# Optimization experiments

Measured on AMD Instinct MI355X. Metric: run time of the kernel, lower is better.

The kernel has to match this reference:

```python
import jax, jax.numpy as jnp
import numpy as np

GAMMA = 0.96875
HIDDEN = 512
BATCH = 4
SEQ = 2048


def setup_inputs() -> dict:
    key = jax.random.key(0)
    k1, k2, k3, k4, k5 = jax.random.split(key, 5)
    x = jax.random.normal(k1, (BATCH, SEQ, HIDDEN), dtype=jnp.float32)
    weight_q = jax.random.normal(k2, (HIDDEN, HIDDEN), dtype=jnp.float32) / HIDDEN
    weight_k = jax.random.normal(k3, (HIDDEN, HIDDEN), dtype=jnp.float32) / HIDDEN
    weight_v = jax.random.normal(k4, (HIDDEN, HIDDEN), dtype=jnp.float32) / HIDDEN
    theta = jax.random.normal(k5, (HIDDEN,), dtype=jnp.float32) / HIDDEN
    return {"x": x, "weight_q": weight_q, "weight_k": weight_k, "weight_v": weight_v, "theta": theta}


def reference(x, weight_q, weight_k, weight_v, theta):
    # x: [B, S, H] float32 -> complex64 parallel retention output [B, S, H]
    B, S, H = x.shape
    cplx = jnp.complex64
    # thetas[n-1] = exp(i * n * theta), n = 1..S  -> [S, H]
    n = jnp.arange(1, S + 1, dtype=jnp.float32)
    phase = n[:, None] * theta[None, :]
    thetas = jnp.exp(1j * phase.astype(cplx))
    xc = x.astype(cplx)
    q = (xc @ weight_q.astype(cplx)) * thetas[None]          # [B, S, H]
    k = (xc @ weight_k.astype(cplx)) * jnp.conj(thetas)[None]
    v = xc @ weight_v.astype(cplx)
    # decay mask D[i, j] = gamma^(i - j) for i >= j else 0   -> [S, S]
    idx = jnp.arange(S)
    diff = idx[:, None] - idx[None, :]
    D = jnp.where(diff >= 0, GAMMA ** jnp.maximum(diff, 0).astype(jnp.float32), 0.0)
    scores = jnp.einsum("bqh,bkh->bqk", q, k) * D.astype(cplx)  # [B, S, S] complex64
    out = jnp.einsum("bqk,bkh->bqh", scores, v)                 # [B, S, H] complex64
    return out
```

## Files before the change

### kernel.cpp

```cpp
#include <hip/hip_runtime.h>
#include <stdint.h>

#define LOG2G -0.045803689611862786f

typedef float f32x4 __attribute__((ext_vector_type(4)));
typedef short bf16x8 __attribute__((ext_vector_type(8)));

__device__ inline unsigned short f2bf(float f) {
  uint32_t u = __builtin_bit_cast(uint32_t, f);
  u += 0x7FFFu + ((u >> 16) & 1u);
  return (unsigned short)(u >> 16);
}
__device__ inline float b2f(unsigned short u) {
  return __builtin_bit_cast(float, (uint32_t)u << 16);
}

#if __has_builtin(__builtin_amdgcn_global_load_lds)
#define USE_GLL 1
#endif

__device__ __forceinline__ void stage_row(const unsigned short* __restrict__ srcrow,
                                          unsigned short* ldsrow, int lane, int swz) {
#ifdef USE_GLL
  __builtin_amdgcn_global_load_lds(
      (const __attribute__((address_space(1))) uint32_t*)((const char*)srcrow + ((lane ^ swz) << 4)),
      (__attribute__((address_space(3))) uint32_t*)ldsrow, 16, 0, 0);
#else
  bf16x8 v = *(const bf16x8*)((const char*)srcrow + ((lane ^ swz) << 4));
  *(bf16x8*)((char*)ldsrow + (lane << 4)) = v;
#endif
}

__global__ __launch_bounds__(256) void prep_kernel(
    const float* __restrict__ wq, const float* __restrict__ wk,
    const float* __restrict__ wv, unsigned short* __restrict__ Wt)
{
  __shared__ unsigned short lh[64][68];
  const int blk = blockIdx.x;
  const int w3 = blk >> 6;
  const int tile = blk & 63;
  const int tk = (tile >> 3) * 64, tn = (tile & 7) * 64;
  const float* W = (w3 == 0) ? wq : ((w3 == 1) ? wk : wv);
  const int t = threadIdx.x;
  {
    const int kl = t >> 2, nq = (t & 3) * 16;
#pragma unroll
    for (int f = 0; f < 4; ++f) {
      float4 v = *(const float4*)&W[(size_t)(tk + kl) * 512 + tn + nq + f * 4];
      float vv[4] = {v.x, v.y, v.z, v.w};
      ushort4 h4;
#pragma unroll
      for (int e = 0; e < 4; ++e) ((unsigned short*)&h4)[e] = f2bf(vv[e]);
      *(ushort4*)&lh[kl][nq + f * 4] = h4;
    }
  }
  __syncthreads();
  {
    const int nl = t >> 2, kq = (t & 3) * 16;
    unsigned short* outh = Wt + (size_t)w3 * 262144 + (size_t)(tn + nl) * 512 + tk + kq;
#pragma unroll
    for (int f = 0; f < 4; ++f) {
      ushort4 h4;
#pragma unroll
      for (int e = 0; e < 4; ++e) ((unsigned short*)&h4)[e] = lh[kq + f * 4 + e][nl];
      *(ushort4*)&outh[f * 4] = h4;
    }
  }
}

__global__ __launch_bounds__(256) void xconv_kernel(
    const float* __restrict__ x, unsigned short* __restrict__ xb)
{
  const size_t i = ((size_t)blockIdx.x * 256 + threadIdx.x) * 8;
  float4 v0 = *(const float4*)&x[i];
  float4 v1 = *(const float4*)&x[i + 4];
  bf16x8 o;
  o[0] = (short)f2bf(v0.x); o[1] = (short)f2bf(v0.y);
  o[2] = (short)f2bf(v0.z); o[3] = (short)f2bf(v0.w);
  o[4] = (short)f2bf(v1.x); o[5] = (short)f2bf(v1.y);
  o[6] = (short)f2bf(v1.z); o[7] = (short)f2bf(v1.w);
  *(bf16x8*)&xb[i] = o;
}

__global__ __launch_bounds__(256) void proj_kernel(
    const unsigned short* __restrict__ xb, const unsigned short* __restrict__ Wt,
    const float* __restrict__ theta,
    unsigned short* __restrict__ Qc, unsigned short* __restrict__ Qs,
    unsigned short* __restrict__ Kc, unsigned short* __restrict__ Ks,
    unsigned short* __restrict__ Vt)
{
  __shared__ unsigned short Al[64 * 512];
  __shared__ unsigned short Bl[64 * 512];
  __shared__ unsigned short T[64][136];
  const int tid = threadIdx.x;
  const int wave = tid >> 6, lane = tid & 63;
  const int r = lane & 15, g = lane >> 4;
  const int wm = wave >> 1, wn = wave & 1;
  const int nbase = blockIdx.x * 64, mbase = blockIdx.y * 64;

#pragma unroll
  for (int i = 0; i < 16; ++i) {
    const int row = wave * 16 + i;
    stage_row(xb + (size_t)(mbase + row) * 512, &Al[row * 512], lane, row & 7);
  }
#pragma unroll
  for (int i = 0; i < 16; ++i) {
    const int row = wave * 16 + i;
    stage_row(Wt + (size_t)(nbase + row) * 512, &Bl[row * 512], lane, row & 7);
  }

  float C1[2], S1[2], CZ[2], SZ[2], C16[2], S16[2];
  const int pos0 = (mbase & 2047) + wm * 32 + g * 4;
#pragma unroll
  for (int nf = 0; nf < 2; ++nf) {
    const float th = theta[nbase + wn * 32 + nf * 16 + r];
    float c1, s1, cz, sz;
    sincosf(th, &s1, &c1);
    sincosf((float)(pos0 + 1) * th, &sz, &cz);
    float c2 = c1 * c1 - s1 * s1, s2 = 2.f * c1 * s1;
    float c4 = c2 * c2 - s2 * s2, s4 = 2.f * c2 * s2;
    float c8 = c4 * c4 - s4 * s4, s8 = 2.f * c4 * s4;
    C1[nf] = c1; S1[nf] = s1; CZ[nf] = cz; SZ[nf] = sz;
    C16[nf] = c8 * c8 - s8 * s8; S16[nf] = 2.f * c8 * s8;
  }
  __syncthreads();

#pragma unroll
  for (int z = 0; z < 3; ++z) {
    f32x4 acc[2][2];
#pragma unroll
    for (int mf = 0; mf < 2; ++mf)
#pragma unroll
      for (int nf = 0; nf < 2; ++nf) acc[mf][nf] = (f32x4){0.f, 0.f, 0.f, 0.f};
#pragma unroll
    for (int ks = 0; ks < 16; ++ks) {
      const int off = (((ks * 4) + g) ^ (r & 7)) << 3;
      bf16x8 a0 = *(const bf16x8*)&Al[(wm * 32 + r) * 512 + off];
      bf16x8 a1 = *(const bf16x8*)&Al[(wm * 32 + 16 + r) * 512 + off];
      bf16x8 b0 = *(const bf16x8*)&Bl[(wn * 32 + r) * 512 + off];
      bf16x8 b1 = *(const bf16x8*)&Bl[(wn * 32 + 16 + r) * 512 + off];
      acc[0][0] = __builtin_amdgcn_mfma_f32_16x16x32_bf16(a0, b0, acc[0][0], 0, 0, 0);
      acc[0][1] = __builtin_amdgcn_mfma_f32_16x16x32_bf16(a0, b1, acc[0][1], 0, 0, 0);
      acc[1][0] = __builtin_amdgcn_mfma_f32_16x16x32_bf16(a1, b0, acc[1][0], 0, 0, 0);
      acc[1][1] = __builtin_amdgcn_mfma_f32_16x16x32_bf16(a1, b1, acc[1][1], 0, 0, 0);
    }
    __syncthreads();

    if (z < 2) {
#pragma unroll
      for (int i = 0; i < 16; ++i) {
        const int row = wave * 16 + i;
        stage_row(Wt + (size_t)(z + 1) * 262144 + (size_t)(nbase + row) * 512,
                  &Bl[row * 512], lane, row & 7);
      }
    }

    if (z == 2) {
#pragma unroll
      for (int nf = 0; nf < 2; ++nf) {
        const int nl = wn * 32 + nf * 16 + r;
#pragma unroll
        for (int mf = 0; mf < 2; ++mf)
#pragma unroll
          for (int i = 0; i < 4; ++i)
            T[nl][wm * 32 + mf * 16 + g * 4 + i] = f2bf(acc[mf][nf][i]);
      }
      __syncthreads();
      const int bb = mbase >> 11, posb = mbase & 2047;
#pragma unroll
      for (int p = 0; p < 2; ++p) {
        const int row = p * 32 + (tid >> 3);
        bf16x8 v = *(const bf16x8*)&T[row][(tid & 7) * 8];
        *(bf16x8*)&Vt[((size_t)bb * 512 + nbase + row) * 2048 + posb + (tid & 7) * 8] = v;
      }
    } else {
#pragma unroll
      for (int pl = 0; pl < 2; ++pl) {
        if (pl) __syncthreads();
#pragma unroll
        for (int nf = 0; nf < 2; ++nf) {
          const int nl = wn * 32 + nf * 16 + r;
          float cz = CZ[nf], sz = SZ[nf];
          const float c1 = C1[nf], s1 = S1[nf], c16 = C16[nf], s16 = S16[nf];
#pragma unroll
          for (int mf = 0; mf < 2; ++mf) {
            float cc = cz, ss = sz;
#pragma unroll
            for (int i = 0; i < 4; ++i) {
              const float f = pl ? ss : cc;
              T[wm * 32 + mf * 16 + g * 4 + i][nl] = f2bf(acc[mf][nf][i] * f);
              float nc = cc * c1 - ss * s1, ns = cc * s1 + ss * c1;
              cc = nc; ss = ns;
            }
            float zc = cz * c16 - sz * s16, zs = cz * s16 + sz * c16;
            cz = zc; sz = zs;
          }
        }
        __syncthreads();
        unsigned short* dst = (z == 0) ? (pl ? Qs : Qc) : (pl ? Ks : Kc);
#pragma unroll
        for (int p = 0; p < 2; ++p) {
          const int row = p * 32 + (tid >> 3);
          bf16x8 v = *(const bf16x8*)&T[row][(tid & 7) * 8];
          *(bf16x8*)&dst[(size_t)(mbase + row) * 512 + nbase + (tid & 7) * 8] = v;
        }
      }
      __syncthreads();
    }
  }
}

__global__ __launch_bounds__(256, 1) void ret_kernel(
    const unsigned short* __restrict__ Qc, const unsigned short* __restrict__ Qs,
    const unsigned short* __restrict__ Kc, const unsigned short* __restrict__ Ks,
    const unsigned short* __restrict__ Vt, uint32_t* __restrict__ out)
{
  __shared__ unsigned short Klds[64 * 512];
  __shared__ unsigned short Prl[2][16 * 40];
  __shared__ unsigned short Pil[2][16 * 40];

  const int bid = blockIdx.x;
  const int sid = ((bid & 7) << 5) + (bid >> 3);
  const int b = sid >> 6;
  const int qblk = 63 - (sid & 63);
  const int q0 = qblk * 32;
  const int tid = threadIdx.x;
  const int wave = tid >> 6;
  const int lane = tid & 63;
  const int r = lane & 15;
  const int g = lane >> 4;
  const int mf = wave & 1;
  const int wq = wave >> 1;
  const int sw = r & 7;

  bf16x8 qa[16], qb[16];
  {
    const unsigned short* qcr = Qc + ((size_t)b * 2048 + q0 + wq * 16 + r) * 512 + g * 8;
    const unsigned short* qsr = Qs + ((size_t)b * 2048 + q0 + wq * 16 + r) * 512 + g * 8;
#pragma unroll
    for (int ks = 0; ks < 16; ++ks) {
      qa[ks] = *(const bf16x8*)(qcr + ks * 32);
      qb[ks] = *(const bf16x8*)(qsr + ks * 32);
    }
  }
#pragma unroll
  for (int ks = 0; ks < 16; ++ks)
    asm volatile("" : "+v"(qa[ks]), "+v"(qb[ks]));

  const int ntiles = ((q0 + 31) >> 5) + 1;
  const int t0 = (q0 >= 256) ? ((q0 - 256) >> 5) : 0;

  {
    const size_t kbase = ((size_t)b * 2048 + (t0 << 5)) * 512;
#pragma unroll
    for (int i = 0; i < 16; ++i) {
      const int rid = wave * 16 + i;
      const int row = rid & 31;
      const unsigned short* src = ((rid < 32) ? Kc : Ks) + kbase + (size_t)row * 512;
      stage_row(src, &Klds[(size_t)rid * 512], lane, rid & 7);
    }
  }
  __syncthreads();

  f32x4 outre[2][8], outim[2][8];
#pragma unroll
  for (int qg = 0; qg < 2; ++qg)
#pragma unroll
    for (int c = 0; c < 8; ++c) {
      outre[qg][c] = (f32x4){0.f, 0.f, 0.f, 0.f};
      outim[qg][c] = (f32x4){0.f, 0.f, 0.f, 0.f};
    }

  for (int t = t0; t < ntiles; ++t) {
    const int m0 = t << 5;
    f32x4 acc_cc = {0.f, 0.f, 0.f, 0.f};
    f32x4 acc_ss = {0.f, 0.f, 0.f, 0.f};
    f32x4 ai1 = {0.f, 0.f, 0.f, 0.f};
    f32x4 ai2 = {0.f, 0.f, 0.f, 0.f};
    const unsigned short* krow_c = &Klds[(mf * 16 + r) * 512];
    const unsigned short* krow_s = krow_c + 32 * 512;
#pragma unroll
    for (int ks = 0; ks < 16; ++ks) {
      const int off = (((ks * 4) + g) ^ sw) << 3;
      bf16x8 ka = *(const bf16x8*)(krow_c + off);
      bf16x8 kb = *(const bf16x8*)(krow_s + off);
      acc_cc = __builtin_amdgcn_mfma_f32_16x16x32_bf16(ka, qa[ks], acc_cc, 0, 0, 0);
      acc_ss = __builtin_amdgcn_mfma_f32_16x16x32_bf16(kb, qb[ks], acc_ss, 0, 0, 0);
      ai1    = __builtin_amdgcn_mfma_f32_16x16x32_bf16(ka, qb[ks], ai1, 0, 0, 0);
      ai2    = __builtin_amdgcn_mfma_f32_16x16x32_bf16(kb, qa[ks], ai2, 0, 0, 0);
    }
    {
      const int qrow = q0 + wq * 16 + r;
      const int mg = m0 + mf * 16 + g * 4;
      ushort4 pkre, pkim;
#pragma unroll
      for (int rg = 0; rg < 4; ++rg) {
        int d = qrow - (mg + rg);
        float wdec = (d >= 0) ? exp2f((float)d * LOG2G) : 0.0f;
        ((unsigned short*)&pkre)[rg] = f2bf((acc_cc[rg] + acc_ss[rg]) * wdec);
        ((unsigned short*)&pkim)[rg] = f2bf((ai1[rg] - ai2[rg]) * wdec);
      }
      *(ushort4*)&Prl[wq][r * 40 + mf * 16 + g * 4] = pkre;
      *(ushort4*)&Pil[wq][r * 40 + mf * 16 + g * 4] = pkim;
    }
    __syncthreads();

    const unsigned short* vtp =
        Vt + ((size_t)b * 512 + wave * 128 + r) * 2048 + m0 + g * 8;
    bf16x8 vv[8];
#pragma unroll
    for (int c = 0; c < 8; ++c)
      vv[c] = *(const bf16x8*)(vtp + (size_t)c * 16 * 2048);

    if (t + 1 < ntiles) {
      const size_t kbase = ((size_t)b * 2048 + m0 + 32) * 512;
#pragma unroll
      for (int i = 0; i < 16; ++i) {
        const int rid = wave * 16 + i;
        const int row = rid & 31;
        const unsigned short* src = ((rid < 32) ? Kc : Ks) + kbase + (size_t)row * 512;
        stage_row(src, &Klds[(size_t)rid * 512], lane, rid & 7);
      }
    }

#pragma unroll
    for (int qg = 0; qg < 2; ++qg) {
      bf16x8 pr = *(const bf16x8*)&Prl[qg][r * 40 + g * 8];
      bf16x8 pi = *(const bf16x8*)&Pil[qg][r * 40 + g * 8];
#pragma unroll
      for (int c = 0; c < 8; ++c) {
        outre[qg][c] = __builtin_amdgcn_mfma_f32_16x16x32_bf16(pr, vv[c], outre[qg][c], 0, 0, 0);
        outim[qg][c] = __builtin_amdgcn_mfma_f32_16x16x32_bf16(pi, vv[c], outim[qg][c], 0, 0, 0);
      }
    }
    __syncthreads();
  }

#pragma unroll
  for (int qg = 0; qg < 2; ++qg)
#pragma unroll
    for (int c = 0; c < 8; ++c)
#pragma unroll
      for (int rg = 0; rg < 4; ++rg) {
        const int q = q0 + qg * 16 + g * 4 + rg;
        const int h = wave * 128 + c * 16 + r;
        const size_t o = ((size_t)b * 2048 + q) * 512 + h;
        out[o] = (uint32_t)f2bf(outim[qg][c][rg]) | ((uint32_t)f2bf(outre[qg][c][rg]) << 16);
      }
}

extern "C" void kernel_launch(void* const* d_in, const int* in_sizes, int n_in,
                              void* d_out, int out_size, void* d_ws, size_t ws_size,
                              hipStream_t stream) {
  (void)in_sizes; (void)n_in; (void)out_size; (void)ws_size;
  const float* x     = (const float*)d_in[0];
  const float* wq    = (const float*)d_in[1];
  const float* wk    = (const float*)d_in[2];
  const float* wv    = (const float*)d_in[3];
  const float* theta = (const float*)d_in[4];

  const size_t NEL = (size_t)4 * 2048 * 512;
  unsigned short* Qc = (unsigned short*)d_ws;
  unsigned short* Qs = Qc + NEL;
  unsigned short* Kc = Qs + NEL;
  unsigned short* Ks = Kc + NEL;
  unsigned short* Vt = Ks + NEL;
  unsigned short* Wt = (unsigned short*)d_out;
  unsigned short* xb = (unsigned short*)d_out + 2097152;

  prep_kernel<<<192, 256, 0, stream>>>(wq, wk, wv, Wt);
  xconv_kernel<<<2048, 256, 0, stream>>>(x, xb);
  dim3 gp(8, 128);
  proj_kernel<<<gp, 256, 0, stream>>>(xb, Wt, theta, Qc, Qs, Kc, Ks, Vt);
  ret_kernel<<<256, 256, 0, stream>>>(Qc, Qs, Kc, Ks, Vt, (uint32_t*)d_out);
}
```

Baseline: 96.74 us.

## Restructure projection kernel to stream weight tiles with double buffering per row block

The projection kernel now runs one block per 32-row slice of x, kept resident in LDS, and loops over all 48 weight tiles (Q, K, V × 16). Each next weight tile is staged into a second LDS buffer while the current one is multiplied. This cuts the grid from 1024 to 256 blocks, reading x only once and overlapping weight loads with MFMA work. In exchange, each wave holds a single 16x16 accumulator, there are more barriers and sincos calls per tile, and V is written with narrower 8-byte stores, which may lower MFMA utilization.

```diff
diff --git a/kernel.cpp b/kernel.cpp
--- a/kernel.cpp
+++ b/kernel.cpp
@@ -82,127 +82,91 @@
   *(bf16x8*)&xb[i] = o;
 }
 
-__global__ __launch_bounds__(256) void proj_kernel(
+__global__ __launch_bounds__(256, 1) void proj_kernel(
     const unsigned short* __restrict__ xb, const unsigned short* __restrict__ Wt,
     const float* __restrict__ theta,
     unsigned short* __restrict__ Qc, unsigned short* __restrict__ Qs,
     unsigned short* __restrict__ Kc, unsigned short* __restrict__ Ks,
     unsigned short* __restrict__ Vt)
 {
-  __shared__ unsigned short Al[64 * 512];
-  __shared__ unsigned short Bl[64 * 512];
-  __shared__ unsigned short T[64][136];
+  __shared__ unsigned short Al[32 * 512];
+  __shared__ unsigned short Bl[2][32 * 512];
+  __shared__ unsigned short Tc[32][72];
+  __shared__ unsigned short Ts[32][72];
   const int tid = threadIdx.x;
   const int wave = tid >> 6, lane = tid & 63;
   const int r = lane & 15, g = lane >> 4;
   const int wm = wave >> 1, wn = wave & 1;
-  const int nbase = blockIdx.x * 64, mbase = blockIdx.y * 64;
-
-#pragma unroll
-  for (int i = 0; i < 16; ++i) {
-    const int row = wave * 16 + i;
+  const int mbase = blockIdx.x * 32;
+  const int b = mbase >> 11;
+  const int posb = mbase & 2047;
+
+#pragma unroll
+  for (int i = 0; i < 8; ++i) {
+    const int row = wave * 8 + i;
     stage_row(xb + (size_t)(mbase + row) * 512, &Al[row * 512], lane, row & 7);
   }
 #pragma unroll
-  for (int i = 0; i < 16; ++i) {
-    const int row = wave * 16 + i;
-    stage_row(Wt + (size_t)(nbase + row) * 512, &Bl[row * 512], lane, row & 7);
-  }
-
-  float C1[2], S1[2], CZ[2], SZ[2], C16[2], S16[2];
-  const int pos0 = (mbase & 2047) + wm * 32 + g * 4;
-#pragma unroll
-  for (int nf = 0; nf < 2; ++nf) {
-    const float th = theta[nbase + wn * 32 + nf * 16 + r];
-    float c1, s1, cz, sz;
-    sincosf(th, &s1, &c1);
-    sincosf((float)(pos0 + 1) * th, &sz, &cz);
-    float c2 = c1 * c1 - s1 * s1, s2 = 2.f * c1 * s1;
-    float c4 = c2 * c2 - s2 * s2, s4 = 2.f * c2 * s2;
-    float c8 = c4 * c4 - s4 * s4, s8 = 2.f * c4 * s4;
-    C1[nf] = c1; S1[nf] = s1; CZ[nf] = cz; SZ[nf] = sz;
-    C16[nf] = c8 * c8 - s8 * s8; S16[nf] = 2.f * c8 * s8;
+  for (int i = 0; i < 8; ++i) {
+    const int row = wave * 8 + i;
+    stage_row(Wt + (size_t)row * 512, &Bl[0][row * 512], lane, row & 7);
   }
   __syncthreads();
 
-#pragma unroll
   for (int z = 0; z < 3; ++z) {
-    f32x4 acc[2][2];
-#pragma unroll
-    for (int mf = 0; mf < 2; ++mf)
-#pragma unroll
-      for (int nf = 0; nf < 2; ++nf) acc[mf][nf] = (f32x4){0.f, 0.f, 0.f, 0.f};
-#pragma unroll
-    for (int ks = 0; ks < 16; ++ks) {
-      const int off = (((ks * 4) + g) ^ (r & 7)) << 3;
-      bf16x8 a0 = *(const bf16x8*)&Al[(wm * 32 + r) * 512 + off];
-      bf16x8 a1 = *(const bf16x8*)&Al[(wm * 32 + 16 + r) * 512 + off];
-      bf16x8 b0 = *(const bf16x8*)&Bl[(wn * 32 + r) * 512 + off];
-      bf16x8 b1 = *(const bf16x8*)&Bl[(wn * 32 + 16 + r) * 512 + off];
-      acc[0][0] = __builtin_amdgcn_mfma_f32_16x16x32_bf16(a0, b0, acc[0][0], 0, 0, 0);
-      acc[0][1] = __builtin_amdgcn_mfma_f32_16x16x32_bf16(a0, b1, acc[0][1], 0, 0, 0);
-      acc[1][0] = __builtin_amdgcn_mfma_f32_16x16x32_bf16(a1, b0, acc[1][0], 0, 0, 0);
-      acc[1][1] = __builtin_amdgcn_mfma_f32_16x16x32_bf16(a1, b1, acc[1][1], 0, 0, 0);
-    }
-    __syncthreads();
-
-    if (z < 2) {
-#pragma unroll
-      for (int i = 0; i < 16; ++i) {
-        const int row = wave * 16 + i;
-        stage_row(Wt + (size_t)(z + 1) * 262144 + (size_t)(nbase + row) * 512,
-                  &Bl[row * 512], lane, row & 7);
-      }
-    }
-
-    if (z == 2) {
-#pragma unroll
-      for (int nf = 0; nf < 2; ++nf) {
-        const int nl = wn * 32 + nf * 16 + r;
-#pragma unroll
-        for (int mf = 0; mf < 2; ++mf)
-#pragma unroll
-          for (int i = 0; i < 4; ++i)
-            T[nl][wm * 32 + mf * 16 + g * 4 + i] = f2bf(acc[mf][nf][i]);
-      }
-      __syncthreads();
-      const int bb = mbase >> 11, posb = mbase & 2047;
-#pragma unroll
-      for (int p = 0; p < 2; ++p) {
-        const int row = p * 32 + (tid >> 3);
-        bf16x8 v = *(const bf16x8*)&T[row][(tid & 7) * 8];
-        *(bf16x8*)&Vt[((size_t)bb * 512 + nbase + row) * 2048 + posb + (tid & 7) * 8] = v;
-      }
-    } else {
-#pragma unroll
-      for (int pl = 0; pl < 2; ++pl) {
-        if (pl) __syncthreads();
-#pragma unroll
-        for (int nf = 0; nf < 2; ++nf) {
-          const int nl = wn * 32 + nf * 16 + r;
-          float cz = CZ[nf], sz = SZ[nf];
-          const float c1 = C1[nf], s1 = S1[nf], c16 = C16[nf], s16 = S16[nf];
-#pragma unroll
-          for (int mf = 0; mf < 2; ++mf) {
-            float cc = cz, ss = sz;
-#pragma unroll
-            for (int i = 0; i < 4; ++i) {
-              const float f = pl ? ss : cc;
-              T[wm * 32 + mf * 16 + g * 4 + i][nl] = f2bf(acc[mf][nf][i] * f);
-              float nc = cc * c1 - ss * s1, ns = cc * s1 + ss * c1;
-              cc = nc; ss = ns;
-            }
-            float zc = cz * c16 - sz * s16, zs = cz * s16 + sz * c16;
-            cz = zc; sz = zs;
-          }
+    for (int nt = 0; nt < 16; ++nt) {
+      const int s = z * 16 + nt;
+      const int cur = s & 1;
+
+      if (s + 1 < 48) {
+        const int zn = (s + 1) >> 4, ntn = (s + 1) & 15;
+#pragma unroll
+        for (int i = 0; i < 8; ++i) {
+          const int row = wave * 8 + i;
+          stage_row(Wt + (size_t)zn * 262144 + (size_t)(ntn * 32 + row) * 512,
+                    &Bl[cur ^ 1][row * 512], lane, row & 7);
         }
-        __syncthreads();
-        unsigned short* dst = (z == 0) ? (pl ? Qs : Qc) : (pl ? Ks : Kc);
-#pragma unroll
-        for (int p = 0; p < 2; ++p) {
-          const int row = p * 32 + (tid >> 3);
-          bf16x8 v = *(const bf16x8*)&T[row][(tid & 7) * 8];
-          *(bf16x8*)&dst[(size_t)(mbase + row) * 512 + nbase + (tid & 7) * 8] = v;
+      }
+
+      f32x4 acc = {0.f, 0.f, 0.f, 0.f};
+#pragma unroll
+      for (int ks = 0; ks < 16; ++ks) {
+        const int off = (((ks * 4) + g) ^ (r & 7)) << 3;
+        bf16x8 a = *(const bf16x8*)&Al[(wm * 16 + r) * 512 + off];
+        bf16x8 bb = *(const bf16x8*)&Bl[cur][(wn * 16 + r) * 512 + off];
+        acc = __builtin_amdgcn_mfma_f32_16x16x32_bf16(a, bb, acc, 0, 0, 0);
+      }
+
+      if (z == 2) {
+        const int h = nt * 32 + wn * 16 + r;
+        ushort4 vp;
+#pragma unroll
+        for (int i = 0; i < 4; ++i) ((unsigned short*)&vp)[i] = f2bf(acc[i]);
+        *(ushort4*)&Vt[((size_t)b * 512 + h) * 2048 + posb + wm * 16 + g * 4] = vp;
+      } else {
+        const int n = nt * 32 + wn * 16 + r;
+        const float th = theta[n];
+        float c1, s1, cz, sz;
+        sincosf(th, &s1, &c1);
+        const int pos0 = posb + wm * 16 + g * 4;
+        sincosf((float)(pos0 + 1) * th, &sz, &cz);
+        const int col = (nt & 1) * 32 + wn * 16 + r;
+#pragma unroll
+        for (int i = 0; i < 4; ++i) {
+          const int mrow = wm * 16 + g * 4 + i;
+          Tc[mrow][col] = f2bf(acc[i] * cz);
+          Ts[mrow][col] = f2bf(acc[i] * sz);
+          float nc = cz * c1 - sz * s1, ns = cz * s1 + sz * c1;
+          cz = nc; sz = ns;
+        }
+        if (nt & 1) {
+          __syncthreads();
+          const int row = tid >> 3, c8 = (tid & 7) * 8;
+          const int nb = (nt >> 1) * 64;
+          unsigned short* dc = (z == 0) ? Qc : Kc;
+          unsigned short* ds = (z == 0) ? Qs : Ks;
+          *(bf16x8*)&dc[(size_t)(mbase + row) * 512 + nb + c8] = *(const bf16x8*)&Tc[row][c8];
+          *(bf16x8*)&ds[(size_t)(mbase + row) * 512 + nb + c8] = *(const bf16x8*)&Ts[row][c8];
         }
       }
       __syncthreads();
@@ -370,7 +334,6 @@
 
   prep_kernel<<<192, 256, 0, stream>>>(wq, wk, wv, Wt);
   xconv_kernel<<<2048, 256, 0, stream>>>(x, xb);
-  dim3 gp(8, 128);
-  proj_kernel<<<gp, 256, 0, stream>>>(xb, Wt, theta, Qc, Qs, Kc, Ks, Vt);
+  proj_kernel<<<256, 256, 0, stream>>>(xb, Wt, theta, Qc, Qs, Kc, Ks, Vt);
   ret_kernel<<<256, 256, 0, stream>>>(Qc, Qs, Kc, Ks, Vt, (uint32_t*)d_out);
 }
```

Result: slower. 123.6 us (+27.8%).
